# Performance work log

Hardware: AMD Instinct MI355X
Metric: run time of the kernel (lower is better)

The kernel has to match this reference:

```python
import jax, jax.numpy as jnp
import numpy as np


def conv1x1(x, W, b):
    # x: [B,C,H,W], W: [O,C], b: [O]  (torch Conv2d 1x1 squeezed)
    return jnp.einsum('oc,bchw->bohw', W, x) + b[None, :, None, None]


def setup_inputs() -> dict:
    key = jax.random.key(0)
    ks = jax.random.split(key, 7)
    B, C, H, W = 8, 256, 32, 32
    s = 1.0 / np.sqrt(C)
    x = jax.random.normal(ks[0], (B, C, H, W), jnp.float32)
    Wq = jax.random.normal(ks[1], (C, C), jnp.float32) * s
    bq = jax.random.normal(ks[2], (C,), jnp.float32) * 0.01
    Wk = jax.random.normal(ks[3], (C, C), jnp.float32) * s
    bk = jax.random.normal(ks[4], (C,), jnp.float32) * 0.01
    Wo = jax.random.normal(ks[5], (C, C), jnp.float32) * s
    bo = jax.random.normal(ks[6], (C,), jnp.float32) * 0.01
    return {"x": x, "Wq": Wq, "bq": bq, "Wk": Wk, "bk": bk, "Wo": Wo, "bo": bo}


def reference(x, Wq, bq, Wk, bk, Wo, bo):
    B, C, H, W = x.shape
    HW = H * W
    scale = 1.0 / (C ** 0.5)
    # proj_query: torch does view(B,C,HW).permute(0,2,1).transpose(1,2).contiguous().view(-1,C)
    # which is a row-major reshape of [B,C,HW] into [B*HW, C] (channel/spatial interleaved).
    # Reproduced faithfully.
    q = conv1x1(x, Wq, bq).reshape(B, C, HW).reshape(-1, C)          # [B*HW, C]
    # proj_key: view(B,C,HW).transpose(0,1).contiguous().view(C,-1) -> true [C, B*HW]
    k = jnp.transpose(conv1x1(x, Wk, bk).reshape(B, C, HW), (1, 0, 2)).reshape(C, -1)
    x_w = (q @ k).reshape(B * HW, B, HW)                              # [BHW, B, HW]
    out_co = jnp.max(x_w, axis=-1) + jnp.mean(x_w, axis=-1)           # [BHW, B]
    x_co = jnp.mean(out_co, axis=-1).reshape(B, HW) * scale           # [B, HW]
    x_co = jax.nn.softmax(x_co, axis=-1).reshape(B, 1, H, W)
    return conv1x1(x * x_co, Wo, bo)
```

## Files before the change

kernel.cpp:

```cpp
#include <hip/hip_runtime.h>

#define BATCH 8
#define CH 256
#define HWSZ 1024
#define BHW 8192

typedef _Float16 f16;
typedef _Float16 f16x4 __attribute__((ext_vector_type(4)));
typedef _Float16 f16x8 __attribute__((ext_vector_type(8)));
typedef float f32x4 __attribute__((ext_vector_type(4)));
typedef unsigned long long u64;
typedef __attribute__((address_space(3))) unsigned int lds_u32;
typedef __attribute__((address_space(1))) const unsigned int glob_u32;

__global__ __launch_bounds__(256) void kmeanW_kernel(
    const float* __restrict__ Wk, const float* __restrict__ bk,
    const float* __restrict__ xsum, float* __restrict__ kmean, float* __restrict__ ksum)
{
    __shared__ float xm[BATCH][CH];
    __shared__ float sm[32][8];
    const int tid = threadIdx.x;
#pragma unroll
    for (int i = 0; i < 8; ++i) xm[i][tid] = xsum[i * 256 + tid] * (1.0f / HWSZ);
    __syncthreads();

    const int co = blockIdx.x * 32 + (tid >> 3);
    const int b  = tid & 7;
    float acc = 0.f;
    const float4* w = (const float4*)(Wk + (size_t)co * CH);
    for (int c4 = 0; c4 < 64; ++c4) {
        float4 wv = w[c4];
        acc = fmaf(wv.x, xm[b][c4 * 4 + 0], acc);
        acc = fmaf(wv.y, xm[b][c4 * 4 + 1], acc);
        acc = fmaf(wv.z, xm[b][c4 * 4 + 2], acc);
        acc = fmaf(wv.w, xm[b][c4 * 4 + 3], acc);
    }
    const float v = acc + bk[co];
    kmean[b * 256 + co] = v;
    sm[tid >> 3][b] = v;
    __syncthreads();
    if (tid < 32) {
        float s = 0.f;
#pragma unroll
        for (int j = 0; j < 8; ++j) s += sm[tid][j];
        ksum[blockIdx.x * 32 + tid] = s;
    }
}

__global__ __launch_bounds__(256, 2) void pgemmQKY_kernel(
    const float* __restrict__ x,
    const float* __restrict__ Wq, const float* __restrict__ Wk, const float* __restrict__ Wo,
    const float* __restrict__ bq, const float* __restrict__ bk,
    f16* __restrict__ Qh, char* __restrict__ Ksw, f16* __restrict__ Yh,
    float* __restrict__ xsum)
{
    __shared__ __align__(16) char kbuf[32 * 1024];
    __shared__ __align__(16) float xt[256][36];
    f16* tile = (f16*)&xt[0][0];
    char* tileb = (char*)&xt[0][0];

    const int bid  = blockIdx.x;
    const int h    = bid >> 8;
    const int p    = bid & 255;
    const int pxg0 = p * 32;
    const int b    = pxg0 >> 10;
    const int hw0  = pxg0 & 1023;
    const int tid  = threadIdx.x;
    const int lane = tid & 63;
    const int wid  = tid >> 6;
    const int m = lane & 15, g = lane >> 4;
    const int coW = h * 128;

    {
        const int f4 = tid & 7;
        const int cs = tid >> 3;
#pragma unroll
        for (int pass = 0; pass < 8; ++pass) {
            const int c = pass * 32 + cs;
            float4 v = *(const float4*)(x + ((size_t)b * CH + c) * HWSZ + hw0 + f4 * 4);
            *(float4*)&xt[c][f4 * 4] = v;
        }
    }
    __syncthreads();

    {
        const int px = tid & 31;
        const int q8 = tid >> 5;
        const int sw = (px & 7) << 4;
#pragma unroll
        for (int r = 0; r < 4; ++r) {
            f16x8 hi, lo;
#pragma unroll
            for (int i = 0; i < 8; ++i) {
                const int c = q8 * 32 + r * 8 + i;
                float v = xt[c][px];
                f16 hv = (f16)v;
                hi[i] = hv;
                lo[i] = (f16)(v - (float)hv);
            }
            const int base = q8 * 64 + r * 16;
            *(f16x8*)(kbuf + px * 1024 + (base ^ sw)) = hi;
            *(f16x8*)(kbuf + px * 1024 + 512 + (base ^ sw)) = lo;
        }
    }

    if (h == 0) {
        float s = 0.f;
#pragma unroll
        for (int i4 = 0; i4 < 8; ++i4) {
            float4 v = *(const float4*)&xt[tid][i4 * 4];
            s += v.x + v.y + v.z + v.w;
        }
        atomicAdd(&xsum[b * 256 + tid], s);
    }

    f16x8 a[2][8];
#define LOAD_W(Wsel)                                                                     \
    {                                                                                    \
        _Pragma("unroll")                                                                \
        for (int t = 0; t < 2; ++t)                                                      \
            _Pragma("unroll")                                                            \
            for (int kk = 0; kk < 8; ++kk) {                                             \
                const float* wrow = (Wsel) + (size_t)(coW + wid * 32 + t * 16 + m) * CH + kk * 32 + g * 8; \
                float4 w0 = *(const float4*)(wrow);                                      \
                float4 w1 = *(const float4*)(wrow + 4);                                  \
                f16x8 av;                                                                \
                av[0] = (f16)w0.x; av[1] = (f16)w0.y; av[2] = (f16)w0.z; av[3] = (f16)w0.w; \
                av[4] = (f16)w1.x; av[5] = (f16)w1.y; av[6] = (f16)w1.z; av[7] = (f16)w1.w; \
                a[t][kk] = av;                                                           \
            }                                                                            \
    }
    LOAD_W(Wq);
    __syncthreads();

    const int sw0 = (m & 7) << 4;
    const f32x4 vz = {0.f, 0.f, 0.f, 0.f};
    f32x4 acc[2][2];

#define MFMA_PASS(NKS)                                                                   \
    {                                                                                    \
        _Pragma("unroll")                                                                \
        for (int t = 0; t < 2; ++t) { acc[t][0] = vz; acc[t][1] = vz; }                  \
        _Pragma("unroll")                                                                \
        for (int ks = 0; ks < (NKS); ++ks) {                                             \
            const int X = ks * 64 + g * 16;                                              \
            f16x8 b0 = *(const f16x8*)(kbuf + m * 1024 + (X ^ sw0));                     \
            f16x8 b1 = *(const f16x8*)(kbuf + (16 + m) * 1024 + (X ^ sw0));              \
            _Pragma("unroll")                                                            \
            for (int t = 0; t < 2; ++t) {                                                \
                acc[t][0] = __builtin_amdgcn_mfma_f32_16x16x32_f16(a[t][ks & 7], b0, acc[t][0], 0, 0, 0); \
                acc[t][1] = __builtin_amdgcn_mfma_f32_16x16x32_f16(a[t][ks & 7], b1, acc[t][1], 0, 0, 0); \
            }                                                                            \
        }                                                                                \
    }

    MFMA_PASS(16);
#pragma unroll
    for (int t = 0; t < 2; ++t) {
        const int lco0 = wid * 32 + t * 16 + 4 * g;
        float4 bv = *(const float4*)(bq + coW + lco0);
        float ba[4] = {bv.x, bv.y, bv.z, bv.w};
#pragma unroll
        for (int u = 0; u < 2; ++u) {
            const int px = u * 16 + m;
#pragma unroll
            for (int j = 0; j < 4; ++j)
                tile[(lco0 + j) * 32 + (px ^ (j << 3))] = (f16)(acc[t][u][j] + ba[j]);
        }
    }
    __syncthreads();
#pragma unroll
    for (int pass = 0; pass < 2; ++pass) {
        const int lco = pass * 64 + (tid >> 2);
        const int run = tid & 3;
        f16x8 v = *(const f16x8*)(tile + lco * 32 + ((run * 8) ^ ((lco & 3) << 3)));
        *(f16x8*)(Qh + ((size_t)b * CH + coW + lco) * HWSZ + hw0 + run * 8) = v;
    }

    LOAD_W(Wk);
    MFMA_PASS(16);
    __syncthreads();
#pragma unroll
    for (int t = 0; t < 2; ++t) {
        const int lco0 = wid * 32 + t * 16 + 4 * g;
        float4 bv = *(const float4*)(bk + coW + lco0);
        float ba[4] = {bv.x, bv.y, bv.z, bv.w};
#pragma unroll
        for (int u = 0; u < 2; ++u) {
            const int px = u * 16 + m;
            f16x4 pk;
#pragma unroll
            for (int j = 0; j < 4; ++j) pk[j] = (f16)(acc[t][u][j] + ba[j]);
            *(f16x4*)(tileb + px * 256 + ((lco0 * 2) ^ (m << 3))) = pk;
        }
    }
    __syncthreads();
    {
        const int px = tid & 31;
        const int rp = tid >> 5;
        const int kloc = (px & 15) << 3;
        const int kglb = (px & 7) << 4;
        char* grow = Ksw + (size_t)(pxg0 + px) * 512 + h * 256;
#pragma unroll
        for (int i = 0; i < 2; ++i) {
            const int rl = rp + i * 8;
            u64 a0 = *(const u64*)(tileb + px * 256 + ((rl * 16) ^ kloc));
            u64 a1 = *(const u64*)(tileb + px * 256 + ((rl * 16 + 8) ^ kloc));
            char* gdst = grow + ((rl * 16) ^ kglb);
            *(u64*)gdst = a0;
            *(u64*)(gdst + 8) = a1;
        }
    }

    LOAD_W(Wo);
    MFMA_PASS(8);
    __syncthreads();
#pragma unroll
    for (int t = 0; t < 2; ++t) {
        const int lco0 = wid * 32 + t * 16 + 4 * g;
#pragma unroll
        for (int u = 0; u < 2; ++u) {
            const int px = u * 16 + m;
#pragma unroll
            for (int j = 0; j < 4; ++j)
                tile[(lco0 + j) * 32 + (px ^ (j << 3))] = (f16)acc[t][u][j];
        }
    }
    __syncthreads();
#pragma unroll
    for (int pass = 0; pass < 2; ++pass) {
        const int lco = pass * 64 + (tid >> 2);
        const int run = tid & 3;
        f16x8 v = *(const f16x8*)(tile + lco * 32 + ((run * 8) ^ ((lco & 3) << 3)));
        *(f16x8*)(Yh + ((size_t)b * CH + coW + lco) * HWSZ + hw0 + run * 8) = v;
    }
#undef MFMA_PASS
#undef LOAD_W
}

__global__ __launch_bounds__(256, 2) void score_kernel(
    const f16* __restrict__ Qh, const char* __restrict__ Ksw,
    const float* __restrict__ ksum, float* __restrict__ rowdq, float* __restrict__ rowq)
{
    __shared__ __align__(16) char kbuf[2][32768];
    __shared__ float lds_rm[128][2];
    __shared__ float lds_dq[128];
    __shared__ float kmS[CH];

    const int batch = blockIdx.x & 7;
    const int r0    = (blockIdx.x >> 3) * 128;
    const int tid   = threadIdx.x;
    const int lane  = tid & 63;
    const int wid   = tid >> 6;
    const int wr = wid >> 1, wc = wid & 1;
    const int m = lane & 15, g = lane >> 4;
    const int rbase = r0 + wr * 64;

    if (batch == 0) kmS[tid] = ksum[tid];

    const char* kbase = Ksw + (size_t)batch * HWSZ * 512;

#define STAGE(buf, ch)                                                                   \
    {                                                                                    \
        const char* _src = kbase + (ch) * 64 * 512 + tid * 16;                           \
        char* _dst = &kbuf[buf][tid * 16];                                               \
        _Pragma("unroll")                                                                \
        for (int k = 0; k < 8; ++k)                                                      \
            __builtin_amdgcn_global_load_lds((glob_u32*)(_src + k * 4096),               \
                                             (lds_u32*)(_dst + k * 4096), 16, 0, 0);     \
    }

    STAGE(0, 0);

    f16x8 a[4][8];
#pragma unroll
    for (int t = 0; t < 4; ++t)
#pragma unroll
        for (int kk = 0; kk < 8; ++kk)
            a[t][kk] = *(const f16x8*)(Qh + (size_t)(rbase + t * 16 + m) * CH + kk * 32 + 8 * g);
#pragma unroll
    for (int t = 0; t < 4; ++t)
#pragma unroll
        for (int kk = 0; kk < 8; ++kk)
            asm volatile("" : "+v"(a[t][kk]));

    int Ebase[2];
    {
        const int low = ((g * 16) ^ ((m & 3) << 4)) + (((m >> 2) & 1) << 6);
#pragma unroll
        for (int u2 = 0; u2 < 2; ++u2)
            Ebase[u2] = (wc * 32 + u2 * 16 + m) * 512 + low;
    }

    float rm[4][4];
#pragma unroll
    for (int t = 0; t < 4; ++t)
#pragma unroll
        for (int jj = 0; jj < 4; ++jj) rm[t][jj] = -1e30f;

    int cur = 0;
    for (int ch = 0; ch < 16; ++ch) {
        if (ch < 15) {
            STAGE(cur ^ 1, ch + 1);
            asm volatile("s_waitcnt vmcnt(8)" ::: "memory");
        } else {
            asm volatile("s_waitcnt vmcnt(0)" ::: "memory");
        }
        __builtin_amdgcn_s_barrier();

        const char* kb = &kbuf[cur][0];
        f32x4 acc[4][2];
        const f32x4 vz = {0.f, 0.f, 0.f, 0.f};
#pragma unroll
        for (int t = 0; t < 4; ++t) { acc[t][0] = vz; acc[t][1] = vz; }

#pragma unroll
        for (int kk = 0; kk < 8; ++kk) {
            f16x8 bfr[2];
            const int xorb = (kk & 1) << 6;
            const int imm  = (kk >> 1) * 128;
            bfr[0] = *(const f16x8*)(kb + (Ebase[0] ^ xorb) + imm);
            bfr[1] = *(const f16x8*)(kb + (Ebase[1] ^ xorb) + imm);
#pragma unroll
            for (int t = 0; t < 4; ++t) {
                acc[t][0] = __builtin_amdgcn_mfma_f32_16x16x32_f16(a[t][kk], bfr[0], acc[t][0], 0, 0, 0);
                acc[t][1] = __builtin_amdgcn_mfma_f32_16x16x32_f16(a[t][kk], bfr[1], acc[t][1], 0, 0, 0);
            }
        }

#pragma unroll
        for (int t = 0; t < 4; ++t)
#pragma unroll
            for (int jj = 0; jj < 4; ++jj)
                rm[t][jj] = fmaxf(rm[t][jj], fmaxf(acc[t][0][jj], acc[t][1][jj]));

        asm volatile("" ::: "memory");
        __builtin_amdgcn_s_barrier();
        cur ^= 1;
    }
#undef STAGE

#pragma unroll
    for (int d = 1; d < 16; d <<= 1)
#pragma unroll
        for (int t = 0; t < 4; ++t)
#pragma unroll
            for (int jj = 0; jj < 4; ++jj)
                rm[t][jj] = fmaxf(rm[t][jj], __shfl_xor(rm[t][jj], d, 64));

    if (m == 0) {
#pragma unroll
        for (int t = 0; t < 4; ++t)
#pragma unroll
            for (int jj = 0; jj < 4; ++jj)
                lds_rm[wr * 64 + t * 16 + g * 4 + jj][wc] = rm[t][jj];
    }

    if (batch == 0) {
        float dq[4];
#pragma unroll
        for (int t = 0; t < 4; ++t) {
            float s = 0.f;
#pragma unroll
            for (int kk = 0; kk < 8; ++kk)
#pragma unroll
                for (int i = 0; i < 8; ++i)
                    s = fmaf((float)a[t][kk][i], kmS[kk * 32 + 8 * g + i], s);
            s += __shfl_xor(s, 16, 64);
            s += __shfl_xor(s, 32, 64);
            dq[t] = s;
        }
        if (wc == 0 && lane < 16) {
#pragma unroll
            for (int t = 0; t < 4; ++t)
                lds_dq[wr * 64 + t * 16 + lane] = dq[t];
        }
        __syncthreads();
        if (tid < 128) {
            rowq[r0 + tid] = lds_dq[tid];
            rowdq[(size_t)(r0 + tid) * 8] = fmaxf(lds_rm[tid][0], lds_rm[tid][1]);
        }
    } else {
        __syncthreads();
        if (tid < 128)
            rowdq[(size_t)(r0 + tid) * 8 + batch] = fmaxf(lds_rm[tid][0], lds_rm[tid][1]);
    }
}

__global__ __launch_bounds__(256) void softmax_kernel(const float* __restrict__ rowdq,
                                                      const float* __restrict__ rowq,
                                                      float* __restrict__ wgt)
{
    const int br = blockIdx.x, tid = threadIdx.x;
    __shared__ float red[256];
    float l[4];
#pragma unroll
    for (int i = 0; i < 4; ++i) {
        const size_t r = (size_t)br * HWSZ + i * 256 + tid;
        float4 v0 = *(const float4*)(rowdq + r * 8);
        float4 v1 = *(const float4*)(rowdq + r * 8 + 4);
        l[i] = (v0.x + v0.y + v0.z + v0.w + v1.x + v1.y + v1.z + v1.w + rowq[r]) * (1.0f / 128.0f);
    }

    float mx = fmaxf(fmaxf(l[0], l[1]), fmaxf(l[2], l[3]));
    red[tid] = mx;
    __syncthreads();
    for (int s = 128; s > 0; s >>= 1) {
        if (tid < s) red[tid] = fmaxf(red[tid], red[tid + s]);
        __syncthreads();
    }
    mx = red[0];
    __syncthreads();

    float e[4], sm = 0.f;
#pragma unroll
    for (int i = 0; i < 4; ++i) { e[i] = expf(l[i] - mx); sm += e[i]; }
    red[tid] = sm;
    __syncthreads();
    for (int s = 128; s > 0; s >>= 1) {
        if (tid < s) red[tid] += red[tid + s];
        __syncthreads();
    }
    const float inv = 1.0f / red[0];
#pragma unroll
    for (int i = 0; i < 4; ++i)
        wgt[br * HWSZ + i * 256 + tid] = e[i] * inv;
}

__global__ __launch_bounds__(256) void gateY_kernel(const f16* __restrict__ Yh,
                                                    const float* __restrict__ wgt,
                                                    const float* __restrict__ bo,
                                                    float* __restrict__ out)
{
    const size_t idx = ((size_t)blockIdx.x * 256 + threadIdx.x) * 8;
    const int b  = (int)(idx >> 18);
    const int c  = (int)(idx >> 10) & 255;
    const int hw = (int)idx & 1023;

    f16x8 y = *(const f16x8*)(Yh + idx);
    float4 w0 = *(const float4*)(wgt + b * HWSZ + hw);
    float4 w1 = *(const float4*)(wgt + b * HWSZ + hw + 4);
    const float bov = bo[c];

    float4 o0, o1;
    o0.x = fmaf((float)y[0], w0.x, bov); o0.y = fmaf((float)y[1], w0.y, bov);
    o0.z = fmaf((float)y[2], w0.z, bov); o0.w = fmaf((float)y[3], w0.w, bov);
    o1.x = fmaf((float)y[4], w1.x, bov); o1.y = fmaf((float)y[5], w1.y, bov);
    o1.z = fmaf((float)y[6], w1.z, bov); o1.w = fmaf((float)y[7], w1.w, bov);
    *(float4*)(out + idx)     = o0;
    *(float4*)(out + idx + 4) = o1;
}

extern "C" void kernel_launch(void* const* d_in, const int* in_sizes, int n_in,
                              void* d_out, int out_size, void* d_ws, size_t ws_size,
                              hipStream_t stream)
{
    const float* x  = (const float*)d_in[0];
    const float* Wq = (const float*)d_in[1];
    const float* bq = (const float*)d_in[2];
    const float* Wk = (const float*)d_in[3];
    const float* bk = (const float*)d_in[4];
    const float* Wo = (const float*)d_in[5];
    const float* bo = (const float*)d_in[6];
    float* out = (float*)d_out;

    char* ws = (char*)d_ws;
    f16*   Qh     = (f16*)(ws);
    char*  Ksw    = (char*)(ws + (4 << 20));
    f16*   Yh     = (f16*)(ws + (8 << 20));
    float* xsum   = (float*)(ws + (12 << 20));
    float* rowdq  = (float*)(ws + (12 << 20) + (8 << 10));
    float* kmean  = (float*)(ws + (12 << 20) + (264 << 10));
    float* wgt    = (float*)(ws + (12 << 20) + (272 << 10));
    float* ksum   = (float*)(ws + (12 << 20) + (304 << 10));
    float* rowq   = (float*)(ws + (12 << 20) + (308 << 10));

    hipMemsetAsync(xsum, 0, 8 << 10, stream);

    pgemmQKY_kernel<<<dim3(512),  256, 0, stream>>>(x, Wq, Wk, Wo, bq, bk, Qh, Ksw, Yh, xsum);
    kmeanW_kernel  <<<dim3(8),    256, 0, stream>>>(Wk, bk, xsum, kmean, ksum);
    score_kernel   <<<dim3(512),  256, 0, stream>>>(Qh, Ksw, ksum, rowdq, rowq);
    softmax_kernel <<<dim3(8),    256, 0, stream>>>(rowdq, rowq, wgt);
    gateY_kernel   <<<dim3(1024), 256, 0, stream>>>(Yh, wgt, bo, out);
}
```

Before: 87.62 us.

## Widen score kernel to 8 waves with triple-buffered K staging and setprio

```diff
diff --git a/kernel.cpp b/kernel.cpp
--- a/kernel.cpp
+++ b/kernel.cpp
@@ -238,12 +238,12 @@
 #undef LOAD_W
 }
 
-__global__ __launch_bounds__(256, 2) void score_kernel(
+__global__ __launch_bounds__(512, 2) void score_kernel(
     const f16* __restrict__ Qh, const char* __restrict__ Ksw,
     const float* __restrict__ ksum, float* __restrict__ rowdq, float* __restrict__ rowq)
 {
-    __shared__ __align__(16) char kbuf[2][32768];
-    __shared__ float lds_rm[128][2];
+    __shared__ __align__(16) char kbuf[3][32768];
+    __shared__ float lds_rm[128][4];
     __shared__ float lds_dq[128];
     __shared__ float kmS[CH];
 
@@ -252,25 +252,26 @@
     const int tid   = threadIdx.x;
     const int lane  = tid & 63;
     const int wid   = tid >> 6;
-    const int wr = wid >> 1, wc = wid & 1;
+    const int wr = wid >> 2, wc = wid & 3;
     const int m = lane & 15, g = lane >> 4;
     const int rbase = r0 + wr * 64;
 
-    if (batch == 0) kmS[tid] = ksum[tid];
+    if (batch == 0 && tid < 256) kmS[tid] = ksum[tid];
 
     const char* kbase = Ksw + (size_t)batch * HWSZ * 512;
 
 #define STAGE(buf, ch)                                                                   \
     {                                                                                    \
-        const char* _src = kbase + (ch) * 64 * 512 + tid * 16;                           \
-        char* _dst = &kbuf[buf][tid * 16];                                               \
-        _Pragma("unroll")                                                                \
-        for (int k = 0; k < 8; ++k)                                                      \
-            __builtin_amdgcn_global_load_lds((glob_u32*)(_src + k * 4096),               \
-                                             (lds_u32*)(_dst + k * 4096), 16, 0, 0);     \
+        const char* _s = kbase + (ch) * 32768 + tid * 16;                                \
+        char* _d = &kbuf[buf][tid * 16];                                                 \
+        __builtin_amdgcn_global_load_lds((glob_u32*)(_s),          (lds_u32*)(_d),          16, 0, 0); \
+        __builtin_amdgcn_global_load_lds((glob_u32*)(_s +  8192),  (lds_u32*)(_d +  8192),  16, 0, 0); \
+        __builtin_amdgcn_global_load_lds((glob_u32*)(_s + 16384),  (lds_u32*)(_d + 16384),  16, 0, 0); \
+        __builtin_amdgcn_global_load_lds((glob_u32*)(_s + 24576),  (lds_u32*)(_d + 24576),  16, 0, 0); \
     }
 
     STAGE(0, 0);
+    STAGE(1, 1);
 
     f16x8 a[4][8];
 #pragma unroll
@@ -278,65 +279,51 @@
 #pragma unroll
         for (int kk = 0; kk < 8; ++kk)
             a[t][kk] = *(const f16x8*)(Qh + (size_t)(rbase + t * 16 + m) * CH + kk * 32 + 8 * g);
+
+    const int Ebase = (wc * 16 + m) * 512 + (((g * 16) ^ ((m & 3) << 4)) + (((m >> 2) & 1) << 6));
+
+    float rm[4][4];
 #pragma unroll
     for (int t = 0; t < 4; ++t)
 #pragma unroll
-        for (int kk = 0; kk < 8; ++kk)
-            asm volatile("" : "+v"(a[t][kk]));
-
-    int Ebase[2];
-    {
-        const int low = ((g * 16) ^ ((m & 3) << 4)) + (((m >> 2) & 1) << 6);
-#pragma unroll
-        for (int u2 = 0; u2 < 2; ++u2)
-            Ebase[u2] = (wc * 32 + u2 * 16 + m) * 512 + low;
-    }
-
-    float rm[4][4];
-#pragma unroll
-    for (int t = 0; t < 4; ++t)
-#pragma unroll
         for (int jj = 0; jj < 4; ++jj) rm[t][jj] = -1e30f;
 
-    int cur = 0;
+#pragma unroll
     for (int ch = 0; ch < 16; ++ch) {
-        if (ch < 15) {
-            STAGE(cur ^ 1, ch + 1);
+        if (ch < 14) {
+            STAGE((ch + 2) % 3, ch + 2);
             asm volatile("s_waitcnt vmcnt(8)" ::: "memory");
+        } else if (ch == 14) {
+            asm volatile("s_waitcnt vmcnt(4)" ::: "memory");
         } else {
             asm volatile("s_waitcnt vmcnt(0)" ::: "memory");
         }
         __builtin_amdgcn_s_barrier();
 
-        const char* kb = &kbuf[cur][0];
-        f32x4 acc[4][2];
+        const char* kb = &kbuf[ch % 3][0];
+        f32x4 acc[4];
         const f32x4 vz = {0.f, 0.f, 0.f, 0.f};
 #pragma unroll
-        for (int t = 0; t < 4; ++t) { acc[t][0] = vz; acc[t][1] = vz; }
-
+        for (int t = 0; t < 4; ++t) acc[t] = vz;
+
+        __builtin_amdgcn_s_setprio(1);
 #pragma unroll
         for (int kk = 0; kk < 8; ++kk) {
-            f16x8 bfr[2];
-            const int xorb = (kk & 1) << 6;
-            const int imm  = (kk >> 1) * 128;
-            bfr[0] = *(const f16x8*)(kb + (Ebase[0] ^ xorb) + imm);
-            bfr[1] = *(const f16x8*)(kb + (Ebase[1] ^ xorb) + imm);
-#pragma unroll
-            for (int t = 0; t < 4; ++t) {
-                acc[t][0] = __builtin_amdgcn_mfma_f32_16x16x32_f16(a[t][kk], bfr[0], acc[t][0], 0, 0, 0);
-                acc[t][1] = __builtin_amdgcn_mfma_f32_16x16x32_f16(a[t][kk], bfr[1], acc[t][1], 0, 0, 0);
-            }
-        }
+            f16x8 bf = *(const f16x8*)(kb + (Ebase ^ ((kk & 1) << 6)) + (kk >> 1) * 128);
+#pragma unroll
+            for (int t = 0; t < 4; ++t)
+                acc[t] = __builtin_amdgcn_mfma_f32_16x16x32_f16(a[t][kk], bf, acc[t], 0, 0, 0);
+        }
+        __builtin_amdgcn_s_setprio(0);
 
 #pragma unroll
         for (int t = 0; t < 4; ++t)
 #pragma unroll
             for (int jj = 0; jj < 4; ++jj)
-                rm[t][jj] = fmaxf(rm[t][jj], fmaxf(acc[t][0][jj], acc[t][1][jj]));
+                rm[t][jj] = fmaxf(rm[t][jj], acc[t][jj]);
 
         asm volatile("" ::: "memory");
         __builtin_amdgcn_s_barrier();
-        cur ^= 1;
     }
 #undef STAGE
 
@@ -356,7 +343,7 @@
                 lds_rm[wr * 64 + t * 16 + g * 4 + jj][wc] = rm[t][jj];
     }
 
-    if (batch == 0) {
+    if (batch == 0 && wc == 0) {
         float dq[4];
 #pragma unroll
         for (int t = 0; t < 4; ++t) {
@@ -370,20 +357,23 @@
             s += __shfl_xor(s, 32, 64);
             dq[t] = s;
         }
-        if (wc == 0 && lane < 16) {
+        if (lane < 16) {
 #pragma unroll
             for (int t = 0; t < 4; ++t)
                 lds_dq[wr * 64 + t * 16 + lane] = dq[t];
         }
-        __syncthreads();
-        if (tid < 128) {
+    }
+    __syncthreads();
+
+    if (tid < 128) {
+        const float mx = fmaxf(fmaxf(lds_rm[tid][0], lds_rm[tid][1]),
+                               fmaxf(lds_rm[tid][2], lds_rm[tid][3]));
+        if (batch == 0) {
             rowq[r0 + tid] = lds_dq[tid];
-            rowdq[(size_t)(r0 + tid) * 8] = fmaxf(lds_rm[tid][0], lds_rm[tid][1]);
-        }
-    } else {
-        __syncthreads();
-        if (tid < 128)
-            rowdq[(size_t)(r0 + tid) * 8 + batch] = fmaxf(lds_rm[tid][0], lds_rm[tid][1]);
+            rowdq[(size_t)(r0 + tid) * 8] = mx;
+        } else {
+            rowdq[(size_t)(r0 + tid) * 8 + batch] = mx;
+        }
     }
 }
 
@@ -479,7 +469,7 @@
 
     pgemmQKY_kernel<<<dim3(512),  256, 0, stream>>>(x, Wq, Wk, Wo, bq, bk, Qh, Ksw, Yh, xsum);
     kmeanW_kernel  <<<dim3(8),    256, 0, stream>>>(Wk, bk, xsum, kmean, ksum);
-    score_kernel   <<<dim3(512),  256, 0, stream>>>(Qh, Ksw, ksum, rowdq, rowq);
+    score_kernel   <<<dim3(512),  512, 0, stream>>>(Qh, Ksw, ksum, rowdq, rowq);
     softmax_kernel <<<dim3(8),    256, 0, stream>>>(rowdq, rowq, wgt);
     gateY_kernel   <<<dim3(1024), 256, 0, stream>>>(Yh, wgt, bo, out);
 }
```

Measured after the change: 100.2 us. +14.3%, slower.
